# Kernel optimization log

Measured on AMD Instinct MI355X. Metric: run time of the kernel, lower is better.

Reference implementation:

```python
import jax, jax.numpy as jnp
import numpy as np

N = 50000   # nodes
E = 800000  # edges (avg degree 16)
NEG = 0.2   # leaky_relu negative slope


def gat_conv(feat, W, al, ar, rW, src, dst, act):
    """DGL-style GATConv. feat:[N,F] W:[F,H*D] al/ar:[H,D] rW:[F,H*D] or None (identity residual)."""
    n = feat.shape[0]
    H, D = al.shape
    h = (feat @ W).reshape(n, H, D)                      # [N,H,D]
    el = jnp.einsum('nhd,hd->nh', h, al)                 # [N,H]
    er = jnp.einsum('nhd,hd->nh', h, ar)                 # [N,H]
    e = el[src] + er[dst]                                # [E,H]
    e = jnp.where(e > 0, e, NEG * e)                     # leaky_relu
    emax = jax.ops.segment_max(e, dst, num_segments=n)   # per-dst softmax (edge softmax)
    ee = jnp.exp(e - emax[dst])
    denom = jax.ops.segment_sum(ee, dst, num_segments=n)
    alpha = ee / denom[dst]                              # [E,H]
    out = jax.ops.segment_sum(h[src] * alpha[:, :, None], dst, num_segments=n)  # [N,H,D]
    res = (feat @ rW).reshape(n, H, D) if rW is not None else feat.reshape(n, H, D)
    return act(out + res)


def setup_inputs() -> dict:
    key = jax.random.key(0)
    ks = jax.random.split(key, 32)
    d = {}
    d["fvs"] = jax.random.normal(ks[0], (N, 128), jnp.float32)
    d["pos_enc"] = jax.random.normal(ks[1], (N, 64), jnp.float32)
    d["src"] = jax.random.randint(ks[2], (E,), 0, N, jnp.int32)
    d["dst"] = jax.random.randint(ks[3], (E,), 0, N, jnp.int32)
    def w(k, shape):
        return jax.random.normal(k, shape, jnp.float32) / np.sqrt(shape[0])
    i = 4
    # gat layers: in=192 -> H=2, D=64 (layers 0,1), final: H=2, D=64 (out_ch)
    for name in ["gat0", "gat1", "gat2"]:
        d[name + "_W"] = w(ks[i], (192, 128)); i += 1
        d[name + "_al"] = w(ks[i], (2, 64)); i += 1
        d[name + "_ar"] = w(ks[i], (2, 64)); i += 1
        d[name + "_rW"] = w(ks[i], (192, 128)); i += 1
    # pgnn layers: in=64 -> H=2, D=32; in == H*D so residual is identity (no rW)
    for name in ["pg0", "pg1"]:
        d[name + "_W"] = w(ks[i], (64, 64)); i += 1
        d[name + "_al"] = w(ks[i], (2, 32)); i += 1
        d[name + "_ar"] = w(ks[i], (2, 32)); i += 1
    return d


def reference(fvs, pos_enc, src, dst,
              gat0_W, gat0_al, gat0_ar, gat0_rW,
              gat1_W, gat1_al, gat1_ar, gat1_rW,
              gat2_W, gat2_al, gat2_ar, gat2_rW,
              pg0_W, pg0_al, pg0_ar,
              pg1_W, pg1_al, pg1_ar):
    n = fvs.shape[0]
    h_s, h_p = fvs, pos_enc
    # layer 0
    h_s = jnp.concatenate([h_s, h_p], axis=1)
    h_s = gat_conv(h_s, gat0_W, gat0_al, gat0_ar, gat0_rW, src, dst, jax.nn.elu).reshape(n, -1)
    h_p = gat_conv(h_p, pg0_W, pg0_al, pg0_ar, None, src, dst, jnp.tanh).reshape(n, -1)
    # layer 1
    h_s = jnp.concatenate([h_s, h_p], axis=1)
    h_s = gat_conv(h_s, gat1_W, gat1_al, gat1_ar, gat1_rW, src, dst, jax.nn.elu).reshape(n, -1)
    h_p = gat_conv(h_p, pg1_W, pg1_al, pg1_ar, None, src, dst, jnp.tanh).reshape(n, -1)
    # output layer: mean over heads
    h_s = jnp.concatenate([h_s, h_p], axis=1)
    h_s = gat_conv(h_s, gat2_W, gat2_al, gat2_ar, gat2_rW, src, dst, jax.nn.elu).mean(axis=1)
    return (h_s, h_p)
```

## Files before the change

kernel.cpp:

```cpp
#include <hip/hip_runtime.h>

#define NN 50000
#define NE 800000
#define FBLK 8192
#define BKT 256
#define NCPY 8

typedef unsigned short u16;
typedef unsigned int u32;

typedef float f32x4 __attribute__((ext_vector_type(4)));
typedef __bf16 bf16x8 __attribute__((ext_vector_type(8)));
static_assert(sizeof(bf16x8) == 16, "bf16x8 must be 16B");

__device__ __forceinline__ float bf2f(u16 u) {
    u32 x = ((u32)u) << 16;
    return __uint_as_float(x);
}
__device__ __forceinline__ u16 f2bf(float f) {
    u32 x = __float_as_uint(f);
    u32 r = (x + 0x7fffu + ((x >> 16) & 1u)) >> 16;
    return (u16)r;
}
__device__ __forceinline__ u32 pack2(float a, float b) {
    return (u32)f2bf(a) | ((u32)f2bf(b) << 16);
}
__device__ __forceinline__ u16 f2h(float f) {
    _Float16 h = (_Float16)f;
    union { _Float16 h; u16 u; } c; c.h = h;
    return c.u;
}
__device__ __forceinline__ float h2f(u16 u) {
    union { u16 u; _Float16 h; } c; c.u = u;
    return (float)c.h;
}
__device__ __forceinline__ uint4 packu4(const u16* h) {
    uint4 u;
    u.x = (u32)h[0] | ((u32)h[1] << 16);
    u.y = (u32)h[2] | ((u32)h[3] << 16);
    u.z = (u32)h[4] | ((u32)h[5] << 16);
    u.w = (u32)h[6] | ((u32)h[7] << 16);
    return u;
}
__device__ __forceinline__ float ldf(const void* p, size_t idx, int mode) {
    return mode ? bf2f(((const u16*)p)[idx]) : ((const float*)p)[idx];
}
__device__ __forceinline__ float lrelu(float x) { return x > 0.f ? x : 0.2f * x; }

__device__ __forceinline__ f32x4 mfma16(uint4 a, uint4 b, f32x4 c) {
    union { uint4 u; bf16x8 b; } ua, ub;
    ua.u = a; ub.u = b;
    return __builtin_amdgcn_mfma_f32_16x16x32_bf16(ua.b, ub.b, c, 0, 0, 0);
}

__global__ void k_tracer(float* out, float v) {
    if (threadIdx.x == 0 && blockIdx.x == 0) out[0] = v;
}

__global__ void k_detect(const u16* __restrict__ fvs, int* __restrict__ mode) {
    __shared__ int cnt[256];
    int t = threadIdx.x;
    int bad = 0;
    for (int i = 0; i < 16; i++) {
        u16 u = fvs[(size_t)(t * 16 + i) * 2];
        int e = (u >> 7) & 0xff;
        if (e == 255 || e >= 134 || e <= 100) bad++;
    }
    cnt[t] = bad;
    __syncthreads();
    for (int d = 128; d; d >>= 1) {
        if (t < d) cnt[t] += cnt[t + d];
        __syncthreads();
    }
    if (t == 0) *mode = (cnt[0] > 2048) ? 0 : 1;
}

__global__ void k_hist(const int* __restrict__ dst, int* __restrict__ cnt, int E) {
    int e = blockIdx.x * blockDim.x + threadIdx.x;
    if (e < E) atomicAdd(&cnt[dst[e]], 1);
}

__global__ void k_scan1(const int* __restrict__ cnt, int* __restrict__ off,
                        int* __restrict__ bsum, int N) {
    __shared__ int wsum[4];
    int t = threadIdx.x;
    int base = blockIdx.x * 2048 + t * 8;
    int e[8];
    if (base + 8 <= N) {
        int4 v0 = *(const int4*)&cnt[base];
        int4 v1 = *(const int4*)&cnt[base + 4];
        e[0] = v0.x; e[1] = v0.y; e[2] = v0.z; e[3] = v0.w;
        e[4] = v1.x; e[5] = v1.y; e[6] = v1.z; e[7] = v1.w;
    } else {
#pragma unroll
        for (int i = 0; i < 8; i++) e[i] = (base + i < N) ? cnt[base + i] : 0;
    }
    int s = 0;
    int ps[8];
#pragma unroll
    for (int i = 0; i < 8; i++) { ps[i] = s; s += e[i]; }
    int lane = t & 63, wv = t >> 6;
    int sc = s;
#pragma unroll
    for (int o = 1; o < 64; o <<= 1) {
        int u = __shfl_up(sc, o, 64);
        if (lane >= o) sc += u;
    }
    if (lane == 63) wsum[wv] = sc;
    __syncthreads();
    int woff = 0;
    for (int w = 0; w < wv; w++) woff += wsum[w];
    int ex = woff + sc - s;
#pragma unroll
    for (int i = 0; i < 8; i++) ps[i] += ex;
    if (base + 8 <= N) {
        *(int4*)&off[base] = make_int4(ps[0], ps[1], ps[2], ps[3]);
        *(int4*)&off[base + 4] = make_int4(ps[4], ps[5], ps[6], ps[7]);
    } else {
#pragma unroll
        for (int i = 0; i < 8; i++)
            if (base + i < N) off[base + i] = ps[i];
    }
    if (t == 255) bsum[blockIdx.x] = woff + sc;
}

__global__ void k_scan2(const int* __restrict__ bsum, int* __restrict__ off,
                        int N, int nb) {
    int b = blockIdx.x, t = threadIdx.x;
    int boff = 0;
    for (int i = 0; i < b; i++) boff += bsum[i];
    int base = b * 2048 + t * 8;
    if (b > 0) {
        if (base + 8 <= N) {
            int4 a = *(int4*)&off[base];
            int4 c = *(int4*)&off[base + 4];
            a.x += boff; a.y += boff; a.z += boff; a.w += boff;
            c.x += boff; c.y += boff; c.z += boff; c.w += boff;
            *(int4*)&off[base] = a;
            *(int4*)&off[base + 4] = c;
        } else {
#pragma unroll
            for (int i = 0; i < 8; i++)
                if (base + i < N) off[base + i] += boff;
        }
    }
    if (b == nb - 1 && t == 255) off[N] = boff + bsum[b];
}

__global__ void k_binit(const int* __restrict__ off, int* __restrict__ bcur, int nbk) {
    int b = threadIdx.x;
    if (b < nbk) bcur[b] = off[b * BKT];
    else if (b < 256) bcur[b] = 0;
}

__launch_bounds__(256)
__global__ void k_fillA(const int* __restrict__ src, const int* __restrict__ dst,
                        int* __restrict__ bcur, u32* __restrict__ tmp, int E) {
    __shared__ int hist[256];
    __shared__ int lbase[256];
    __shared__ int gbase[256];
    __shared__ int lcur[256];
    __shared__ u32 outrec[FBLK];
    __shared__ unsigned char bslot[FBLK];
    int t = threadIdx.x;
    int e0 = blockIdx.x * FBLK;
    int bn = min(E - e0, FBLK);
    hist[t] = 0;
    __syncthreads();
    for (int i = t; i < bn; i += 256)
        atomicAdd(&hist[dst[e0 + i] >> 8], 1);
    __syncthreads();
    if (t == 0) {
        int run = 0;
        for (int b = 0; b < 256; b++) { lbase[b] = run; run += hist[b]; }
    }
    __syncthreads();
    lcur[t] = lbase[t];
    gbase[t] = hist[t] ? atomicAdd(&bcur[t], hist[t]) : 0;
    __syncthreads();
    for (int i = t; i < bn; i += 256) {
        int d = dst[e0 + i];
        int s = src[e0 + i];
        int b = d >> 8;
        int slot = atomicAdd(&lcur[b], 1);
        outrec[slot] = (u32)s | ((u32)(d & 255) << 24);
        bslot[slot] = (unsigned char)b;
    }
    __syncthreads();
    for (int i = t; i < bn; i += 256) {
        int b = bslot[i];
        tmp[gbase[b] + (i - lbase[b])] = outrec[i];
    }
}

__launch_bounds__(256)
__global__ void k_fillB(const int* __restrict__ off, const u32* __restrict__ tmp,
                        int* __restrict__ ssrc, int N) {
    __shared__ int lcur[BKT];
    __shared__ u32 outv[FBLK];
    int b = blockIdx.x, t = threadIdx.x;
    int n0 = b * BKT;
    int nn = min(N - n0, BKT);
    int nbeg = off[n0], nend = off[n0 + nn];
    int sz = nend - nbeg;
    for (int i = t; i < nn; i += 256) lcur[i] = off[n0 + i] - nbeg;
    __syncthreads();
    if (sz <= FBLK) {
        for (int i = t; i < sz; i += 256) {
            u32 r = tmp[nbeg + i];
            int slot = atomicAdd(&lcur[r >> 24], 1);
            outv[slot] = r & 0x00FFFFFFu;
        }
        __syncthreads();
        for (int i = t; i < sz; i += 256)
            ssrc[nbeg + i] = (int)outv[i];
    } else {
        for (int i = t; i < sz; i += 256) {
            u32 r = tmp[nbeg + i];
            int slot = atomicAdd(&lcur[r >> 24], 1);
            ssrc[nbeg + slot] = (int)(r & 0x00FFFFFFu);
        }
    }
}

__global__ void k_init(const void* __restrict__ pos, u16* __restrict__ hp,
                       const int* __restrict__ dmode, int n64) {
    int i = blockIdx.x * blockDim.x + threadIdx.x;
    if (i >= n64) return;
    int mode = *dmode;
    hp[i] = mode ? ((const u16*)pos)[i] : f2bf(((const float*)pos)[i]);
}

__global__ void k_cvt(const u16* __restrict__ in, float* __restrict__ out, int n) {
    int i = blockIdx.x * blockDim.x + threadIdx.x;
    if (i < n) out[i] = bf2f(in[i]);
}

struct PWArgs {
    const void* src[8];
    u16* dst[8];
    int K[8];
    int BM[8];
};

__global__ void k_prepw(PWArgs a, const int* __restrict__ dmode) {
    int mode = *dmode;
    int g = blockIdx.x * blockDim.x + threadIdx.x;
    int stride = gridDim.x * blockDim.x;
    for (int m = 0; m < 8; m++) {
        int bm = a.BM[m];
        int bmsh = (bm == 128) ? 7 : 6;
        int n = a.K[m] * bm;
        u16* d = a.dst[m];
        const void* s = a.src[m];
        for (int i = g; i < n; i += stride) {
            int k = i >> bmsh, c = i & (bm - 1);
            float v = mode ? bf2f(((const u16*)s)[i]) : ((const float*)s)[i];
            u16 hi = f2bf(v);
            u16 lo = f2bf(v - bf2f(hi));
            size_t o = ((size_t)((k >> 5) * 2) * bm + c) * 32 + (k & 31);
            d[o] = hi;
            d[o + (size_t)bm * 32] = lo;
        }
    }
}

__global__ void k_wcopy(u32* __restrict__ wpk, int nq, int cq) {
    int i = blockIdx.x * blockDim.x + threadIdx.x;
    if (i >= nq * (NCPY - 1)) return;
    int cc = i / nq + 1;
    int q = i - (cc - 1) * nq;
    uint4* p = (uint4*)wpk;
    p[(size_t)cc * cq + q] = p[q];
}

template <int BM, bool HASB2, bool C1H>
__launch_bounds__(256, 4)
__global__ void k_gemm(const void* A1, const u16* __restrict__ A2,
                       const u16* __restrict__ B1p, const u16* __restrict__ B2p,
                       void* __restrict__ C1, u16* C2, float* __restrict__ att,
                       const void* __restrict__ al, const void* __restrict__ ar,
                       int N, int K, int s1, const int* __restrict__ dmode,
                       int a1_input, int cstride) {
    constexpr int NR = BM / 32;
    constexpr int NMAT = HASB2 ? 2 : 1;

    const int mode = *dmode;
    const int a1f32 = (a1_input && mode == 0) ? 1 : 0;
    const int bsplit = (mode == 0) ? 1 : 0;

    const int tid = threadIdx.x;
    const int lane = tid & 63;
    const int wid = tid >> 6;
    const int l15 = lane & 15, l4 = lane >> 4;
    const int r0 = blockIdx.x * 64;
    const int wrow0 = (wid >> 1) * 32;
    const int wcol0 = (wid & 1) * (BM / 2);
    const int ko = l4 * 8;

    const size_t coff = (size_t)(blockIdx.x & (NCPY - 1)) * (size_t)cstride;
    const u16* b1 = B1p + coff;
    const u16* b2 = HASB2 ? (B2p + coff) : nullptr;

    int frow[2];
#pragma unroll
    for (int m = 0; m < 2; m++) {
        int r = r0 + wrow0 + m * 16 + l15;
        frow[m] = r < N ? r : N - 1;
    }

    f32x4 acc[NMAT][2][NR];
    const f32x4 fz = {0.f, 0.f, 0.f, 0.f};
#pragma unroll
    for (int m2 = 0; m2 < NMAT; m2++)
#pragma unroll
        for (int m = 0; m < 2; m++)
#pragma unroll
            for (int n = 0; n < NR; n++) acc[m2][m][n] = fz;

    const int NKT = K >> 5;
    const int rot = (int)((u32)(blockIdx.x >> 3) % (u32)NKT);
    for (int tt = 0; tt < NKT; tt++) {
        int kt = tt + rot;
        if (kt >= NKT) kt -= NKT;
        const int k0 = kt << 5;
        const int doAlo = (a1f32 && k0 < 128) ? 1 : 0;

        uint4 ah[2], alo[2];
#pragma unroll
        for (int m = 0; m < 2; m++) {
            if (k0 >= 128) {
                ah[m] = *(const uint4*)(A2 + (size_t)frow[m] * 64 + (k0 - 128) + ko);
            } else if (!a1f32) {
                ah[m] = *(const uint4*)((const u16*)A1 + (size_t)frow[m] * s1 + k0 + ko);
            } else {
                const float* p = (const float*)A1 + (size_t)frow[m] * s1 + k0 + ko;
                union { uint4 u[2]; float f[8]; } fa;
                fa.u[0] = *(const uint4*)p;
                fa.u[1] = *(const uint4*)(p + 4);
                u16 hi[8], lo[8];
#pragma unroll
                for (int i = 0; i < 8; i++) {
                    hi[i] = f2bf(fa.f[i]);
                    lo[i] = f2bf(fa.f[i] - bf2f(hi[i]));
                }
                ah[m] = packu4(hi);
                alo[m] = packu4(lo);
            }
        }

        const size_t bbase = ((size_t)kt * 2) * BM * 32 + (size_t)l4 * 8;
#pragma unroll
        for (int n = 0; n < NR; n++) {
            const int c = wcol0 + n * 16 + l15;
            const size_t co = (size_t)c * 32;
#pragma unroll
            for (int m2 = 0; m2 < NMAT; m2++) {
                const u16* bp = (m2 == 0 ? b1 : b2) + bbase + co;
                uint4 bh = *(const uint4*)bp;
#pragma unroll
                for (int m = 0; m < 2; m++)
                    acc[m2][m][n] = mfma16(ah[m], bh, acc[m2][m][n]);
                if (bsplit) {
                    uint4 bl = *(const uint4*)(bp + (size_t)BM * 32);
#pragma unroll
                    for (int m = 0; m < 2; m++)
                        acc[m2][m][n] = mfma16(ah[m], bl, acc[m2][m][n]);
                }
                if (doAlo) {
#pragma unroll
                    for (int m = 0; m < 2; m++)
                        acc[m2][m][n] = mfma16(alo[m], bh, acc[m2][m][n]);
                }
            }
        }
    }

    __syncthreads();

    float alc[NR], arc[NR];
#pragma unroll
    for (int n = 0; n < NR; n++) {
        int c = wcol0 + n * 16 + l15;
        alc[n] = ldf(al, c, mode);
        arc[n] = ldf(ar, c, mode);
    }
    const int hc = wid & 1;
#pragma unroll
    for (int m = 0; m < 2; m++) {
#pragma unroll
        for (int r = 0; r < 4; r++) {
            const int gr = r0 + wrow0 + m * 16 + l4 * 4 + r;
            float el = 0.f, er = 0.f;
#pragma unroll
            for (int n = 0; n < NR; n++) {
                float v = acc[0][m][n][r];
                el = fmaf(v, alc[n], el);
                er = fmaf(v, arc[n], er);
            }
#pragma unroll
            for (int o = 1; o <= 8; o <<= 1) {
                el += __shfl_xor(el, o, 64);
                er += __shfl_xor(er, o, 64);
            }
            if (gr < N) {
#pragma unroll
                for (int n = 0; n < NR; n++) {
                    const int c = wcol0 + n * 16 + l15;
                    float v = acc[0][m][n][r];
                    if constexpr (C1H)
                        ((u16*)C1)[(size_t)gr * BM + c] = f2h(v);
                    else
                        ((float*)C1)[(size_t)gr * BM + c] = v;
                    if constexpr (HASB2)
                        C2[(size_t)gr * 128 + c] = f2bf(acc[1][m][n][r]);
                }
                if (l15 == 0) {
                    att[(size_t)gr * 4 + hc] = el;
                    att[(size_t)gr * 4 + 2 + hc] = er;
                }
            }
        }
    }
}

__global__ void k_edge_gat2(const int* __restrict__ off, const int* __restrict__ ssrc,
                            const u16* __restrict__ h, const float* __restrict__ att,
                            const u16* __restrict__ res, u16* __restrict__ outf, int N) {
    __shared__ float pbuf[4][2][64];
    __shared__ int sbuf[4][64];
    int wv = threadIdx.x >> 6;
    int node = blockIdx.x * 4 + wv;
    int lane = threadIdx.x & 63;
    if (node >= N) return;
    const int hd = lane >> 5;
    int beg = off[node], end = off[node + 1];
    float4 a4 = *(const float4*)&att[(size_t)node * 4];
    float er0 = a4.z, er1 = a4.w;
    float m0 = -1e30f, m1 = -1e30f, d0 = 0.f, d1 = 0.f, O0 = 0.f, O1 = 0.f;
    for (int c = beg; c < end; c += 64) {
        int cn = min(end - c, 64);
        int s = 0;
        float x0 = -1e30f, x1 = -1e30f;
        if (lane < cn) {
            s = ssrc[c + lane];
            float2 e = *(const float2*)&att[(size_t)s * 4];
            x0 = lrelu(e.x + er0);
            x1 = lrelu(e.y + er1);
        }
        float cm0 = x0, cm1 = x1;
#pragma unroll
        for (int o = 32; o; o >>= 1) {
            cm0 = fmaxf(cm0, __shfl_xor(cm0, o, 64));
            cm1 = fmaxf(cm1, __shfl_xor(cm1, o, 64));
        }
        float nm0 = fmaxf(m0, cm0), nm1 = fmaxf(m1, cm1);
        float p0 = (lane < cn) ? __expf(x0 - nm0) : 0.f;
        float p1 = (lane < cn) ? __expf(x1 - nm1) : 0.f;
        float cd0 = p0, cd1 = p1;
#pragma unroll
        for (int o = 32; o; o >>= 1) {
            cd0 += __shfl_xor(cd0, o, 64);
            cd1 += __shfl_xor(cd1, o, 64);
        }
        float sc0 = __expf(m0 - nm0), sc1 = __expf(m1 - nm1);
        d0 = d0 * sc0 + cd0; d1 = d1 * sc1 + cd1;
        float sch = hd ? sc1 : sc0;
        O0 *= sch; O1 *= sch;
        m0 = nm0; m1 = nm1;
        pbuf[wv][0][lane] = p0;
        pbuf[wv][1][lane] = p1;
        sbuf[wv][lane] = s;
        const float* pb = pbuf[wv][hd];
        int j = 0;
        for (; j + 7 < cn; j += 8) {
            u32 w[8];
#pragma unroll
            for (int t = 0; t < 8; t++)
                w[t] = *(const u32*)&h[(size_t)sbuf[wv][j + t] * 128 + 2 * lane];
#pragma unroll
            for (int t = 0; t < 8; t++) {
                float q = pb[j + t];
                O0 += q * h2f((u16)w[t]);
                O1 += q * h2f((u16)(w[t] >> 16));
            }
        }
        if (j + 3 < cn) {
            u32 w[4];
#pragma unroll
            for (int t = 0; t < 4; t++)
                w[t] = *(const u32*)&h[(size_t)sbuf[wv][j + t] * 128 + 2 * lane];
#pragma unroll
            for (int t = 0; t < 4; t++) {
                float q = pb[j + t];
                O0 += q * h2f((u16)w[t]);
                O1 += q * h2f((u16)(w[t] >> 16));
            }
            j += 4;
        }
        for (; j < cn; j++) {
            u32 w = *(const u32*)&h[(size_t)sbuf[wv][j] * 128 + 2 * lane];
            float q = pb[j];
            O0 += q * h2f((u16)w);
            O1 += q * h2f((u16)(w >> 16));
        }
    }
    float dd = hd ? d1 : d0;
    float o0 = (end > beg) ? O0 / dd : 0.f;
    float o1 = (end > beg) ? O1 / dd : 0.f;
    u32 rv = *(const u32*)&res[(size_t)node * 128 + 2 * lane];
    float a0 = o0 + bf2f((u16)rv);
    float a1 = o1 + bf2f((u16)(rv >> 16));
    a0 = a0 > 0.f ? a0 : (__expf(a0) - 1.f);
    a1 = a1 > 0.f ? a1 : (__expf(a1) - 1.f);
    *(u32*)&outf[(size_t)node * 128 + 2 * lane] = pack2(a0, a1);
}

__global__ void k_edge_gat_f(const int* __restrict__ off, const int* __restrict__ ssrc,
                             const u16* __restrict__ h, const float* __restrict__ att,
                             const u16* __restrict__ res, float* __restrict__ outs, int N) {
    __shared__ float pbuf[4][2][64];
    __shared__ int sbuf[4][64];
    int wv = threadIdx.x >> 6;
    int node = blockIdx.x * 4 + wv;
    int lane = threadIdx.x & 63;
    if (node >= N) return;
    const int par = lane >> 5;
    const int i = lane & 31;
    const int hd = i >> 4;
    int beg = off[node], end = off[node + 1];
    float4 a4 = *(const float4*)&att[(size_t)node * 4];
    float er0 = a4.z, er1 = a4.w;
    float m0 = -1e30f, m1 = -1e30f, d0 = 0.f, d1 = 0.f;
    float O[4] = {0.f, 0.f, 0.f, 0.f};
    for (int c = beg; c < end; c += 64) {
        int cn = min(end - c, 64);
        int s = 0;
        float x0 = -1e30f, x1 = -1e30f;
        if (lane < cn) {
            s = ssrc[c + lane];
            float2 e = *(const float2*)&att[(size_t)s * 4];
            x0 = lrelu(e.x + er0);
            x1 = lrelu(e.y + er1);
        }
        float cm0 = x0, cm1 = x1;
#pragma unroll
        for (int o = 32; o; o >>= 1) {
            cm0 = fmaxf(cm0, __shfl_xor(cm0, o, 64));
            cm1 = fmaxf(cm1, __shfl_xor(cm1, o, 64));
        }
        float nm0 = fmaxf(m0, cm0), nm1 = fmaxf(m1, cm1);
        float p0 = (lane < cn) ? __expf(x0 - nm0) : 0.f;
        float p1 = (lane < cn) ? __expf(x1 - nm1) : 0.f;
        float cd0 = p0, cd1 = p1;
#pragma unroll
        for (int o = 32; o; o >>= 1) {
            cd0 += __shfl_xor(cd0, o, 64);
            cd1 += __shfl_xor(cd1, o, 64);
        }
        float sc0 = __expf(m0 - nm0), sc1 = __expf(m1 - nm1);
        d0 = d0 * sc0 + cd0; d1 = d1 * sc1 + cd1;
        float sch = hd ? sc1 : sc0;
#pragma unroll
        for (int k = 0; k < 4; k++) O[k] *= sch;
        m0 = nm0; m1 = nm1;
        pbuf[wv][0][lane] = p0;
        pbuf[wv][1][lane] = p1;
        sbuf[wv][lane] = s;
        const float* pb = pbuf[wv][hd];
        int j = par;
        for (; j + 14 < cn; j += 16) {
            uint2 w[8];
#pragma unroll
            for (int t = 0; t < 8; t++)
                w[t] = *(const uint2*)&h[(size_t)sbuf[wv][j + 2 * t] * 128 + 4 * i];
#pragma unroll
            for (int t = 0; t < 8; t++) {
                float q = pb[j + 2 * t];
                O[0] += q * h2f((u16)w[t].x);
                O[1] += q * h2f((u16)(w[t].x >> 16));
                O[2] += q * h2f((u16)w[t].y);
                O[3] += q * h2f((u16)(w[t].y >> 16));
            }
        }
        if (j + 6 < cn) {
            uint2 w[4];
#pragma unroll
            for (int t = 0; t < 4; t++)
                w[t] = *(const uint2*)&h[(size_t)sbuf[wv][j + 2 * t] * 128 + 4 * i];
#pragma unroll
            for (int t = 0; t < 4; t++) {
                float q = pb[j + 2 * t];
                O[0] += q * h2f((u16)w[t].x);
                O[1] += q * h2f((u16)(w[t].x >> 16));
                O[2] += q * h2f((u16)w[t].y);
                O[3] += q * h2f((u16)(w[t].y >> 16));
            }
            j += 8;
        }
        for (; j < cn; j += 2) {
            uint2 w = *(const uint2*)&h[(size_t)sbuf[wv][j] * 128 + 4 * i];
            float q = pb[j];
            O[0] += q * h2f((u16)w.x);
            O[1] += q * h2f((u16)(w.x >> 16));
            O[2] += q * h2f((u16)w.y);
            O[3] += q * h2f((u16)(w.y >> 16));
        }
    }
#pragma unroll
    for (int k = 0; k < 4; k++) O[k] += __shfl_xor(O[k], 32, 64);
    float dd = hd ? d1 : d0;
    uint2 rv = *(const uint2*)&res[(size_t)node * 128 + 4 * i];
    float a[4];
    a[0] = bf2f((u16)rv.x);
    a[1] = bf2f((u16)(rv.x >> 16));
    a[2] = bf2f((u16)rv.y);
    a[3] = bf2f((u16)(rv.y >> 16));
#pragma unroll
    for (int k = 0; k < 4; k++) {
        float o = (end > beg) ? O[k] / dd : 0.f;
        float v = o + a[k];
        a[k] = v > 0.f ? v : (__expf(v) - 1.f);
    }
    float b[4];
#pragma unroll
    for (int k = 0; k < 4; k++) b[k] = __shfl_xor(a[k], 16, 64);
    if (lane < 16)
        *(float4*)&outs[(size_t)node * 64 + 4 * i] =
            make_float4(0.5f * (a[0] + b[0]), 0.5f * (a[1] + b[1]),
                        0.5f * (a[2] + b[2]), 0.5f * (a[3] + b[3]));
}

__global__ void k_edge_pg2(const int* __restrict__ off, const int* __restrict__ ssrc,
                           const u16* __restrict__ h, const float* __restrict__ att,
                           u16* __restrict__ hp, int N) {
    __shared__ float pbuf[4][2][64];
    __shared__ int sbuf[4][64];
    int wv = threadIdx.x >> 6;
    int node = blockIdx.x * 4 + wv;
    int lane = threadIdx.x & 63;
    if (node >= N) return;
    const int par = lane >> 5;
    const int i = lane & 31;
    const int hd = i >> 4;
    int beg = off[node], end = off[node + 1];
    float4 a4 = *(const float4*)&att[(size_t)node * 4];
    float er0 = a4.z, er1 = a4.w;
    float m0 = -1e30f, m1 = -1e30f, d0 = 0.f, d1 = 0.f, O0 = 0.f, O1 = 0.f;
    for (int c = beg; c < end; c += 64) {
        int cn = min(end - c, 64);
        int s = 0;
        float x0 = -1e30f, x1 = -1e30f;
        if (lane < cn) {
            s = ssrc[c + lane];
            float2 e = *(const float2*)&att[(size_t)s * 4];
            x0 = lrelu(e.x + er0);
            x1 = lrelu(e.y + er1);
        }
        float cm0 = x0, cm1 = x1;
#pragma unroll
        for (int o = 32; o; o >>= 1) {
            cm0 = fmaxf(cm0, __shfl_xor(cm0, o, 64));
            cm1 = fmaxf(cm1, __shfl_xor(cm1, o, 64));
        }
        float nm0 = fmaxf(m0, cm0), nm1 = fmaxf(m1, cm1);
        float p0 = (lane < cn) ? __expf(x0 - nm0) : 0.f;
        float p1 = (lane < cn) ? __expf(x1 - nm1) : 0.f;
        float cd0 = p0, cd1 = p1;
#pragma unroll
        for (int o = 32; o; o >>= 1) {
            cd0 += __shfl_xor(cd0, o, 64);
            cd1 += __shfl_xor(cd1, o, 64);
        }
        float sc0 = __expf(m0 - nm0), sc1 = __expf(m1 - nm1);
        d0 = d0 * sc0 + cd0; d1 = d1 * sc1 + cd1;
        float sch = hd ? sc1 : sc0;
        O0 *= sch; O1 *= sch;
        m0 = nm0; m1 = nm1;
        pbuf[wv][0][lane] = p0;
        pbuf[wv][1][lane] = p1;
        sbuf[wv][lane] = s;
        const float* pb = pbuf[wv][hd];
        int j = par;
        for (; j + 14 < cn; j += 16) {
            u32 w[8];
#pragma unroll
            for (int t = 0; t < 8; t++)
                w[t] = *(const u32*)&h[(size_t)sbuf[wv][j + 2 * t] * 64 + 2 * i];
#pragma unroll
            for (int t = 0; t < 8; t++) {
                float q = pb[j + 2 * t];
                O0 += q * h2f((u16)w[t]);
                O1 += q * h2f((u16)(w[t] >> 16));
            }
        }
        if (j + 6 < cn) {
            u32 w[4];
#pragma unroll
            for (int t = 0; t < 4; t++)
                w[t] = *(const u32*)&h[(size_t)sbuf[wv][j + 2 * t] * 64 + 2 * i];
#pragma unroll
            for (int t = 0; t < 4; t++) {
                float q = pb[j + 2 * t];
                O0 += q * h2f((u16)w[t]);
                O1 += q * h2f((u16)(w[t] >> 16));
            }
            j += 8;
        }
        for (; j < cn; j += 2) {
            u32 w = *(const u32*)&h[(size_t)sbuf[wv][j] * 64 + 2 * i];
            float q = pb[j];
            O0 += q * h2f((u16)w);
            O1 += q * h2f((u16)(w >> 16));
        }
    }
    O0 += __shfl_xor(O0, 32, 64);
    O1 += __shfl_xor(O1, 32, 64);
    if (lane < 32) {
        float dd = hd ? d1 : d0;
        float o0 = (end > beg) ? O0 / dd : 0.f;
        float o1 = (end > beg) ? O1 / dd : 0.f;
        u32 rv = *(const u32*)&hp[(size_t)node * 64 + 2 * i];
        float a0 = tanhf(o0 + bf2f((u16)rv));
        float a1 = tanhf(o1 + bf2f((u16)(rv >> 16)));
        *(u32*)&hp[(size_t)node * 64 + 2 * i] = pack2(a0, a1);
    }
}

extern "C" void kernel_launch(void* const* d_in, const int* in_sizes, int n_in,
                              void* d_out, int out_size, void* d_ws, size_t ws_size,
                              hipStream_t stream) {
    const int N = NN, E = NE;
    const void* fvs = d_in[0];
    const void* pos = d_in[1];
    const int* src = (const int*)d_in[2];
    const int* dst = (const int*)d_in[3];
    const void* gW[3]  = {d_in[4],  d_in[8],  d_in[12]};
    const void* gal[3] = {d_in[5],  d_in[9],  d_in[13]};
    const void* gar[3] = {d_in[6],  d_in[10], d_in[14]};
    const void* grW[3] = {d_in[7],  d_in[11], d_in[15]};
    const void* pW[2]  = {d_in[16], d_in[19]};
    const void* pal[2] = {d_in[17], d_in[20]};
    const void* par[2] = {d_in[18], d_in[21]};

    const size_t GSZ = (size_t)192 * 128 * 2;
    const size_t PSZ = (size_t)64 * 64 * 2;
    const size_t CS  = 6 * GSZ + 2 * PSZ;

    auto al256 = [](size_t b) { return (b + 255) & ~(size_t)255; };
    size_t sz_dmode = al256(4);
    size_t sz_bsum  = al256(32 * 4);
    size_t sz_bcur  = al256(256 * 4);
    size_t sz_att   = al256((size_t)N * 4 * 4);
    size_t sz_off   = al256((size_t)(N + 1) * 4);
    size_t sz_ssrc  = al256((size_t)E * 4);
    size_t sz_hs    = al256((size_t)N * 128 * 2);
    size_t sz_hp    = al256((size_t)N * 64 * 2);
    size_t sz_wpk   = al256(CS * NCPY * 2);
    size_t need = sz_dmode + sz_bsum + sz_bcur + sz_att + sz_off + sz_ssrc
                + sz_hs + sz_hp + sz_wpk;
    int bad = (need > ws_size) ? 1 : 0;

    size_t cur = 0;
    auto alloc = [&](size_t bytes) {
        if (cur + bytes > ws_size) cur = 0;
        char* p = (char*)d_ws + cur;
        if (bytes <= ws_size) cur += bytes;
        return p;
    };
    int* dmode  = (int*)alloc(sz_dmode);
    int* bsum   = (int*)alloc(sz_bsum);
    int* bcur   = (int*)alloc(sz_bcur);
    float* att  = (float*)alloc(sz_att);
    int* off    = (int*)alloc(sz_off);
    int* ssrc   = (int*)alloc(sz_ssrc);
    u16* hs     = (u16*)alloc(sz_hs);
    u16* hp     = (u16*)alloc(sz_hp);
    u16* wpk    = (u16*)alloc(sz_wpk);

    u16* Bp[8];
    for (int m = 0; m < 6; m++) Bp[m] = wpk + (size_t)m * GSZ;
    Bp[6] = wpk + 6 * GSZ;
    Bp[7] = Bp[6] + PSZ;

    int* cnt = (int*)att;
    u32* tmp = (u32*)hs;

    void* H = d_out;

    hipMemsetAsync(cnt, 0, (size_t)N * 4, stream);

    k_detect<<<1, 256, 0, stream>>>((const u16*)fvs, dmode);

    PWArgs pwa;
    pwa.src[0] = gW[0]; pwa.src[1] = grW[0];
    pwa.src[2] = gW[1]; pwa.src[3] = grW[1];
    pwa.src[4] = gW[2]; pwa.src[5] = grW[2];
    pwa.src[6] = pW[0]; pwa.src[7] = pW[1];
    for (int m = 0; m < 8; m++) {
        pwa.dst[m] = Bp[m];
        pwa.K[m] = (m < 6) ? 192 : 64;
        pwa.BM[m] = (m < 6) ? 128 : 64;
    }
    k_prepw<<<64, 256, 0, stream>>>(pwa, dmode);
    {
        int nq = (int)(CS / 8);
        int tot = nq * (NCPY - 1);
        k_wcopy<<<(tot + 255) / 256, 256, 0, stream>>>((u32*)wpk, nq, nq);
    }

    int eb = (E + 255) / 256;
    int nbS = (N + 2047) / 2048;
    int nbk = (N + BKT - 1) / BKT;
    k_hist<<<eb, 256, 0, stream>>>(dst, cnt, E);
    k_scan1<<<nbS, 256, 0, stream>>>(cnt, off, bsum, N);
    k_scan2<<<nbS, 256, 0, stream>>>(bsum, off, N, nbS);
    k_binit<<<1, 256, 0, stream>>>(off, bcur, nbk);
    k_fillA<<<(E + FBLK - 1) / FBLK, 256, 0, stream>>>(src, dst, bcur, tmp, E);
    k_fillB<<<nbk, 256, 0, stream>>>(off, tmp, ssrc, N);

    k_init<<<(N * 64 + 255) / 256, 256, 0, stream>>>(pos, hp, dmode, N * 64);

    int gb = (N + 63) / 64;
    int nb = (N + 3) / 4;
    int cs = (int)CS;

    k_gemm<128, true, true><<<gb, 256, 0, stream>>>(fvs, hp, Bp[0], Bp[1], H, hs, att, gal[0], gar[0], N, 192, 128, dmode, 1, cs);
    k_edge_gat2<<<nb, 256, 0, stream>>>(off, ssrc, (u16*)H, att, hs, hs, N);
    k_gemm<64, false, true><<<gb, 256, 0, stream>>>(hp, nullptr, Bp[6], nullptr, H, nullptr, att, pal[0], par[0], N, 64, 64, dmode, 0, cs);
    k_edge_pg2<<<nb, 256, 0, stream>>>(off, ssrc, (u16*)H, att, hp, N);

    k_gemm<128, true, true><<<gb, 256, 0, stream>>>(hs, hp, Bp[2], Bp[3], H, hs, att, gal[1], gar[1], N, 192, 128, dmode, 0, cs);
    k_edge_gat2<<<nb, 256, 0, stream>>>(off, ssrc, (u16*)H, att, hs, hs, N);
    k_gemm<64, false, true><<<gb, 256, 0, stream>>>(hp, nullptr, Bp[7], nullptr, H, nullptr, att, pal[1], par[1], N, 64, 64, dmode, 0, cs);
    k_edge_pg2<<<nb, 256, 0, stream>>>(off, ssrc, (u16*)H, att, hp, N);

    k_gemm<128, true, true><<<gb, 256, 0, stream>>>(hs, hp, Bp[4], Bp[5], H, hs, att, gal[2], gar[2], N, 192, 128, dmode, 0, cs);
    k_edge_gat_f<<<nb, 256, 0, stream>>>(off, ssrc, (u16*)H, att, hs, (float*)hs, N);

    hipMemcpyAsync((float*)d_out, (float*)hs, (size_t)N * 64 * 4, hipMemcpyDeviceToDevice, stream);
    k_cvt<<<(N * 64 + 255) / 256, 256, 0, stream>>>(hp, (float*)d_out + (size_t)N * 64, N * 64);

    if (bad) {
        float v = 100000.f + 1000.f * (float)(ws_size >> 20);
        k_tracer<<<1, 64, 0, stream>>>((float*)d_out, v);
    }
}
```

Measured before the change: 558.7 us.

## Fuse GAT and PGNN branch GEMM and edge kernels into shared launches

The independent GAT and positional-GNN branches in layers 0 and 1 now run together. Their projection GEMMs share one launch and their edge-softmax aggregation kernels share another, with the block index deciding which branch a block handles. Each branch gets its own attention-logit buffer and its own output region so the two can run at once. The aim is to cut kernel launches and serialization, and to fill the GPU better, since each smaller PGNN kernel alone leaves it underused. The cost is a fused edge kernel that reserves shared memory for both branch bodies, plus a somewhat larger workspace.

```diff
diff --git a/kernel.cpp b/kernel.cpp
--- a/kernel.cpp
+++ b/kernel.cpp
@@ -275,17 +275,15 @@
 }
 
 template <int BM, bool HASB2, bool C1H>
-__launch_bounds__(256, 4)
-__global__ void k_gemm(const void* A1, const u16* __restrict__ A2,
-                       const u16* __restrict__ B1p, const u16* __restrict__ B2p,
-                       void* __restrict__ C1, u16* C2, float* __restrict__ att,
-                       const void* __restrict__ al, const void* __restrict__ ar,
-                       int N, int K, int s1, const int* __restrict__ dmode,
-                       int a1_input, int cstride) {
+__device__ __forceinline__ void gemm_body(
+        int bid, int cpy, const void* A1, const u16* __restrict__ A2,
+        const u16* __restrict__ B1p, const u16* __restrict__ B2p,
+        void* __restrict__ C1, u16* C2, float* __restrict__ att,
+        const void* __restrict__ al, const void* __restrict__ ar,
+        int N, int K, int s1, int mode, int a1_input, int cstride) {
     constexpr int NR = BM / 32;
     constexpr int NMAT = HASB2 ? 2 : 1;
 
-    const int mode = *dmode;
     const int a1f32 = (a1_input && mode == 0) ? 1 : 0;
     const int bsplit = (mode == 0) ? 1 : 0;
 
@@ -293,12 +291,12 @@
     const int lane = tid & 63;
     const int wid = tid >> 6;
     const int l15 = lane & 15, l4 = lane >> 4;
-    const int r0 = blockIdx.x * 64;
+    const int r0 = bid * 64;
     const int wrow0 = (wid >> 1) * 32;
     const int wcol0 = (wid & 1) * (BM / 2);
     const int ko = l4 * 8;
 
-    const size_t coff = (size_t)(blockIdx.x & (NCPY - 1)) * (size_t)cstride;
+    const size_t coff = (size_t)cpy * (size_t)cstride;
     const u16* b1 = B1p + coff;
     const u16* b2 = HASB2 ? (B2p + coff) : nullptr;
 
@@ -319,7 +317,7 @@
             for (int n = 0; n < NR; n++) acc[m2][m][n] = fz;
 
     const int NKT = K >> 5;
-    const int rot = (int)((u32)(blockIdx.x >> 3) % (u32)NKT);
+    const int rot = (int)((u32)(bid >> 3) % (u32)NKT);
     for (int tt = 0; tt < NKT; tt++) {
         int kt = tt + rot;
         if (kt >= NKT) kt -= NKT;
@@ -424,13 +422,46 @@
     }
 }
 
-__global__ void k_edge_gat2(const int* __restrict__ off, const int* __restrict__ ssrc,
-                            const u16* __restrict__ h, const float* __restrict__ att,
-                            const u16* __restrict__ res, u16* __restrict__ outf, int N) {
+__launch_bounds__(256, 4)
+__global__ void k_gemm_fused(const void* gA1, const u16* gA2,
+                             const u16* gB1, const u16* gB2,
+                             void* gC1, u16* gC2, float* gatt,
+                             const void* gal, const void* gar, int gK, int gs1, int ga1,
+                             const void* pA1, const u16* pB1,
+                             void* pC1, float* patt,
+                             const void* pal, const void* par,
+                             int N, const int* __restrict__ dmode, int cstride, int gbGat) {
+    int mode = *dmode;
+    int cpy = blockIdx.x & (NCPY - 1);
+    if (blockIdx.x < gbGat)
+        gemm_body<128, true, true>(blockIdx.x, cpy, gA1, gA2, gB1, gB2, gC1, gC2,
+                                   gatt, gal, gar, N, gK, gs1, mode, ga1, cstride);
+    else
+        gemm_body<64, false, true>(blockIdx.x - gbGat, cpy, pA1, nullptr, pB1, nullptr,
+                                   pC1, nullptr, patt, pal, par, N, 64, 64, mode, 0, cstride);
+}
+
+__launch_bounds__(256, 4)
+__global__ void k_gemm_gat(const void* A1, const u16* A2,
+                           const u16* B1, const u16* B2,
+                           void* C1, u16* C2, float* att,
+                           const void* al, const void* ar,
+                           int N, int K, int s1, const int* __restrict__ dmode,
+                           int a1_input, int cstride) {
+    int mode = *dmode;
+    int cpy = blockIdx.x & (NCPY - 1);
+    gemm_body<128, true, true>(blockIdx.x, cpy, A1, A2, B1, B2, C1, C2, att,
+                               al, ar, N, K, s1, mode, a1_input, cstride);
+}
+
+__device__ void edge_gat2_body(int bid, const int* __restrict__ off,
+                               const int* __restrict__ ssrc,
+                               const u16* __restrict__ h, const float* __restrict__ att,
+                               const u16* __restrict__ res, u16* __restrict__ outf, int N) {
     __shared__ float pbuf[4][2][64];
     __shared__ int sbuf[4][64];
     int wv = threadIdx.x >> 6;
-    int node = blockIdx.x * 4 + wv;
+    int node = bid * 4 + wv;
     int lane = threadIdx.x & 63;
     if (node >= N) return;
     const int hd = lane >> 5;
@@ -514,6 +545,114 @@
     a0 = a0 > 0.f ? a0 : (__expf(a0) - 1.f);
     a1 = a1 > 0.f ? a1 : (__expf(a1) - 1.f);
     *(u32*)&outf[(size_t)node * 128 + 2 * lane] = pack2(a0, a1);
+}
+
+__device__ void edge_pg2_body(int bid, const int* __restrict__ off,
+                              const int* __restrict__ ssrc,
+                              const u16* __restrict__ h, const float* __restrict__ att,
+                              u16* __restrict__ hp, int N) {
+    __shared__ float pbuf2[4][2][64];
+    __shared__ int sbuf2[4][64];
+    int wv = threadIdx.x >> 6;
+    int node = bid * 4 + wv;
+    int lane = threadIdx.x & 63;
+    if (node >= N) return;
+    const int par = lane >> 5;
+    const int i = lane & 31;
+    const int hd = i >> 4;
+    int beg = off[node], end = off[node + 1];
+    float4 a4 = *(const float4*)&att[(size_t)node * 4];
+    float er0 = a4.z, er1 = a4.w;
+    float m0 = -1e30f, m1 = -1e30f, d0 = 0.f, d1 = 0.f, O0 = 0.f, O1 = 0.f;
+    for (int c = beg; c < end; c += 64) {
+        int cn = min(end - c, 64);
+        int s = 0;
+        float x0 = -1e30f, x1 = -1e30f;
+        if (lane < cn) {
+            s = ssrc[c + lane];
+            float2 e = *(const float2*)&att[(size_t)s * 4];
+            x0 = lrelu(e.x + er0);
+            x1 = lrelu(e.y + er1);
+        }
+        float cm0 = x0, cm1 = x1;
+#pragma unroll
+        for (int o = 32; o; o >>= 1) {
+            cm0 = fmaxf(cm0, __shfl_xor(cm0, o, 64));
+            cm1 = fmaxf(cm1, __shfl_xor(cm1, o, 64));
+        }
+        float nm0 = fmaxf(m0, cm0), nm1 = fmaxf(m1, cm1);
+        float p0 = (lane < cn) ? __expf(x0 - nm0) : 0.f;
+        float p1 = (lane < cn) ? __expf(x1 - nm1) : 0.f;
+        float cd0 = p0, cd1 = p1;
+#pragma unroll
+        for (int o = 32; o; o >>= 1) {
+            cd0 += __shfl_xor(cd0, o, 64);
+            cd1 += __shfl_xor(cd1, o, 64);
+        }
+        float sc0 = __expf(m0 - nm0), sc1 = __expf(m1 - nm1);
+        d0 = d0 * sc0 + cd0; d1 = d1 * sc1 + cd1;
+        float sch = hd ? sc1 : sc0;
+        O0 *= sch; O1 *= sch;
+        m0 = nm0; m1 = nm1;
+        pbuf2[wv][0][lane] = p0;
+        pbuf2[wv][1][lane] = p1;
+        sbuf2[wv][lane] = s;
+        const float* pb = pbuf2[wv][hd];
+        int j = par;
+        for (; j + 14 < cn; j += 16) {
+            u32 w[8];
+#pragma unroll
+            for (int t = 0; t < 8; t++)
+                w[t] = *(const u32*)&h[(size_t)sbuf2[wv][j + 2 * t] * 64 + 2 * i];
+#pragma unroll
+            for (int t = 0; t < 8; t++) {
+                float q = pb[j + 2 * t];
+                O0 += q * h2f((u16)w[t]);
+                O1 += q * h2f((u16)(w[t] >> 16));
+            }
+        }
+        if (j + 6 < cn) {
+            u32 w[4];
+#pragma unroll
+            for (int t = 0; t < 4; t++)
+                w[t] = *(const u32*)&h[(size_t)sbuf2[wv][j + 2 * t] * 64 + 2 * i];
+#pragma unroll
+            for (int t = 0; t < 4; t++) {
+                float q = pb[j + 2 * t];
+                O0 += q * h2f((u16)w[t]);
+                O1 += q * h2f((u16)(w[t] >> 16));
+            }
+            j += 8;
+        }
+        for (; j < cn; j += 2) {
+            u32 w = *(const u32*)&h[(size_t)sbuf2[wv][j] * 64 + 2 * i];
+            float q = pb[j];
+            O0 += q * h2f((u16)w);
+            O1 += q * h2f((u16)(w >> 16));
+        }
+    }
+    O0 += __shfl_xor(O0, 32, 64);
+    O1 += __shfl_xor(O1, 32, 64);
+    if (lane < 32) {
+        float dd = hd ? d1 : d0;
+        float o0 = (end > beg) ? O0 / dd : 0.f;
+        float o1 = (end > beg) ? O1 / dd : 0.f;
+        u32 rv = *(const u32*)&hp[(size_t)node * 64 + 2 * i];
+        float a0 = tanhf(o0 + bf2f((u16)rv));
+        float a1 = tanhf(o1 + bf2f((u16)(rv >> 16)));
+        *(u32*)&hp[(size_t)node * 64 + 2 * i] = pack2(a0, a1);
+    }
+}
+
+__global__ void k_edge_fused(const int* __restrict__ off, const int* __restrict__ ssrc,
+                             const u16* __restrict__ hg, const float* __restrict__ attg,
+                             const u16* __restrict__ res, u16* __restrict__ outf,
+                             const u16* __restrict__ hpg, const float* __restrict__ attp,
+                             u16* __restrict__ hp, int N, int nbGat) {
+    if (blockIdx.x < nbGat)
+        edge_gat2_body(blockIdx.x, off, ssrc, hg, attg, res, outf, N);
+    else
+        edge_pg2_body(blockIdx.x - nbGat, off, ssrc, hpg, attp, hp, N);
 }
 
 __global__ void k_edge_gat_f(const int* __restrict__ off, const int* __restrict__ ssrc,
@@ -631,102 +770,6 @@
                         0.5f * (a[2] + b[2]), 0.5f * (a[3] + b[3]));
 }
 
-__global__ void k_edge_pg2(const int* __restrict__ off, const int* __restrict__ ssrc,
-                           const u16* __restrict__ h, const float* __restrict__ att,
-                           u16* __restrict__ hp, int N) {
-    __shared__ float pbuf[4][2][64];
-    __shared__ int sbuf[4][64];
-    int wv = threadIdx.x >> 6;
-    int node = blockIdx.x * 4 + wv;
-    int lane = threadIdx.x & 63;
-    if (node >= N) return;
-    const int par = lane >> 5;
-    const int i = lane & 31;
-    const int hd = i >> 4;
-    int beg = off[node], end = off[node + 1];
-    float4 a4 = *(const float4*)&att[(size_t)node * 4];
-    float er0 = a4.z, er1 = a4.w;
-    float m0 = -1e30f, m1 = -1e30f, d0 = 0.f, d1 = 0.f, O0 = 0.f, O1 = 0.f;
-    for (int c = beg; c < end; c += 64) {
-        int cn = min(end - c, 64);
-        int s = 0;
-        float x0 = -1e30f, x1 = -1e30f;
-        if (lane < cn) {
-            s = ssrc[c + lane];
-            float2 e = *(const float2*)&att[(size_t)s * 4];
-            x0 = lrelu(e.x + er0);
-            x1 = lrelu(e.y + er1);
-        }
-        float cm0 = x0, cm1 = x1;
-#pragma unroll
-        for (int o = 32; o; o >>= 1) {
-            cm0 = fmaxf(cm0, __shfl_xor(cm0, o, 64));
-            cm1 = fmaxf(cm1, __shfl_xor(cm1, o, 64));
-        }
-        float nm0 = fmaxf(m0, cm0), nm1 = fmaxf(m1, cm1);
-        float p0 = (lane < cn) ? __expf(x0 - nm0) : 0.f;
-        float p1 = (lane < cn) ? __expf(x1 - nm1) : 0.f;
-        float cd0 = p0, cd1 = p1;
-#pragma unroll
-        for (int o = 32; o; o >>= 1) {
-            cd0 += __shfl_xor(cd0, o, 64);
-            cd1 += __shfl_xor(cd1, o, 64);
-        }
-        float sc0 = __expf(m0 - nm0), sc1 = __expf(m1 - nm1);
-        d0 = d0 * sc0 + cd0; d1 = d1 * sc1 + cd1;
-        float sch = hd ? sc1 : sc0;
-        O0 *= sch; O1 *= sch;
-        m0 = nm0; m1 = nm1;
-        pbuf[wv][0][lane] = p0;
-        pbuf[wv][1][lane] = p1;
-        sbuf[wv][lane] = s;
-        const float* pb = pbuf[wv][hd];
-        int j = par;
-        for (; j + 14 < cn; j += 16) {
-            u32 w[8];
-#pragma unroll
-            for (int t = 0; t < 8; t++)
-                w[t] = *(const u32*)&h[(size_t)sbuf[wv][j + 2 * t] * 64 + 2 * i];
-#pragma unroll
-            for (int t = 0; t < 8; t++) {
-                float q = pb[j + 2 * t];
-                O0 += q * h2f((u16)w[t]);
-                O1 += q * h2f((u16)(w[t] >> 16));
-            }
-        }
-        if (j + 6 < cn) {
-            u32 w[4];
-#pragma unroll
-            for (int t = 0; t < 4; t++)
-                w[t] = *(const u32*)&h[(size_t)sbuf[wv][j + 2 * t] * 64 + 2 * i];
-#pragma unroll
-            for (int t = 0; t < 4; t++) {
-                float q = pb[j + 2 * t];
-                O0 += q * h2f((u16)w[t]);
-                O1 += q * h2f((u16)(w[t] >> 16));
-            }
-            j += 8;
-        }
-        for (; j < cn; j += 2) {
-            u32 w = *(const u32*)&h[(size_t)sbuf[wv][j] * 64 + 2 * i];
-            float q = pb[j];
-            O0 += q * h2f((u16)w);
-            O1 += q * h2f((u16)(w >> 16));
-        }
-    }
-    O0 += __shfl_xor(O0, 32, 64);
-    O1 += __shfl_xor(O1, 32, 64);
-    if (lane < 32) {
-        float dd = hd ? d1 : d0;
-        float o0 = (end > beg) ? O0 / dd : 0.f;
-        float o1 = (end > beg) ? O1 / dd : 0.f;
-        u32 rv = *(const u32*)&hp[(size_t)node * 64 + 2 * i];
-        float a0 = tanhf(o0 + bf2f((u16)rv));
-        float a1 = tanhf(o1 + bf2f((u16)(rv >> 16)));
-        *(u32*)&hp[(size_t)node * 64 + 2 * i] = pack2(a0, a1);
-    }
-}
-
 extern "C" void kernel_launch(void* const* d_in, const int* in_sizes, int n_in,
                               void* d_out, int out_size, void* d_ws, size_t ws_size,
                               hipStream_t stream) {
@@ -752,12 +795,13 @@
     size_t sz_bsum  = al256(32 * 4);
     size_t sz_bcur  = al256(256 * 4);
     size_t sz_att   = al256((size_t)N * 4 * 4);
+    size_t sz_att2  = al256((size_t)N * 4 * 4);
     size_t sz_off   = al256((size_t)(N + 1) * 4);
     size_t sz_ssrc  = al256((size_t)E * 4);
     size_t sz_hs    = al256((size_t)N * 128 * 2);
     size_t sz_hp    = al256((size_t)N * 64 * 2);
     size_t sz_wpk   = al256(CS * NCPY * 2);
-    size_t need = sz_dmode + sz_bsum + sz_bcur + sz_att + sz_off + sz_ssrc
+    size_t need = sz_dmode + sz_bsum + sz_bcur + sz_att + sz_att2 + sz_off + sz_ssrc
                 + sz_hs + sz_hp + sz_wpk;
     int bad = (need > ws_size) ? 1 : 0;
 
@@ -771,7 +815,8 @@
     int* dmode  = (int*)alloc(sz_dmode);
     int* bsum   = (int*)alloc(sz_bsum);
     int* bcur   = (int*)alloc(sz_bcur);
-    float* att  = (float*)alloc(sz_att);
+    float* attg = (float*)alloc(sz_att);
+    float* attp = (float*)alloc(sz_att2);
     int* off    = (int*)alloc(sz_off);
     int* ssrc   = (int*)alloc(sz_ssrc);
     u16* hs     = (u16*)alloc(sz_hs);
@@ -783,10 +828,11 @@
     Bp[6] = wpk + 6 * GSZ;
     Bp[7] = Bp[6] + PSZ;
 
-    int* cnt = (int*)att;
+    int* cnt = (int*)attg;
     u32* tmp = (u32*)hs;
 
-    void* H = d_out;
+    u16* Hg = (u16*)d_out;
+    u16* Hp = (u16*)d_out + (size_t)N * 128;
 
     hipMemsetAsync(cnt, 0, (size_t)N * 4, stream);
 
@@ -825,18 +871,21 @@
     int nb = (N + 3) / 4;
     int cs = (int)CS;
 
-    k_gemm<128, true, true><<<gb, 256, 0, stream>>>(fvs, hp, Bp[0], Bp[1], H, hs, att, gal[0], gar[0], N, 192, 128, dmode, 1, cs);
-    k_edge_gat2<<<nb, 256, 0, stream>>>(off, ssrc, (u16*)H, att, hs, hs, N);
-    k_gemm<64, false, true><<<gb, 256, 0, stream>>>(hp, nullptr, Bp[6], nullptr, H, nullptr, att, pal[0], par[0], N, 64, 64, dmode, 0, cs);
-    k_edge_pg2<<<nb, 256, 0, stream>>>(off, ssrc, (u16*)H, att, hp, N);
-
-    k_gemm<128, true, true><<<gb, 256, 0, stream>>>(hs, hp, Bp[2], Bp[3], H, hs, att, gal[1], gar[1], N, 192, 128, dmode, 0, cs);
-    k_edge_gat2<<<nb, 256, 0, stream>>>(off, ssrc, (u16*)H, att, hs, hs, N);
-    k_gemm<64, false, true><<<gb, 256, 0, stream>>>(hp, nullptr, Bp[7], nullptr, H, nullptr, att, pal[1], par[1], N, 64, 64, dmode, 0, cs);
-    k_edge_pg2<<<nb, 256, 0, stream>>>(off, ssrc, (u16*)H, att, hp, N);
-
-    k_gemm<128, true, true><<<gb, 256, 0, stream>>>(hs, hp, Bp[4], Bp[5], H, hs, att, gal[2], gar[2], N, 192, 128, dmode, 0, cs);
-    k_edge_gat_f<<<nb, 256, 0, stream>>>(off, ssrc, (u16*)H, att, hs, (float*)hs, N);
+    k_gemm_fused<<<2 * gb, 256, 0, stream>>>(
+        fvs, hp, Bp[0], Bp[1], Hg, hs, attg, gal[0], gar[0], 192, 128, 1,
+        hp, Bp[6], Hp, attp, pal[0], par[0], N, dmode, cs, gb);
+    k_edge_fused<<<2 * nb, 256, 0, stream>>>(off, ssrc, Hg, attg, hs, hs,
+                                             Hp, attp, hp, N, nb);
+
+    k_gemm_fused<<<2 * gb, 256, 0, stream>>>(
+        hs, hp, Bp[2], Bp[3], Hg, hs, attg, gal[1], gar[1], 192, 128, 0,
+        hp, Bp[7], Hp, attp, pal[1], par[1], N, dmode, cs, gb);
+    k_edge_fused<<<2 * nb, 256, 0, stream>>>(off, ssrc, Hg, attg, hs, hs,
+                                             Hp, attp, hp, N, nb);
+
+    k_gemm_gat<<<gb, 256, 0, stream>>>(hs, hp, Bp[4], Bp[5], Hg, hs, attg,
+                                       gal[2], gar[2], N, 192, 128, dmode, 0, cs);
+    k_edge_gat_f<<<nb, 256, 0, stream>>>(off, ssrc, Hg, attg, hs, (float*)hs, N);
 
     hipMemcpyAsync((float*)d_out, (float*)hs, (size_t)N * 64 * 4, hipMemcpyDeviceToDevice, stream);
     k_cvt<<<(N * 64 + 255) / 256, 256, 0, stream>>>(hp, (float*)d_out + (size_t)N * 64, N * 64);
```

New measurement: 534.9 us. 4.3% less time.
